# Kernel optimization log

Measured on AMD Instinct MI355X. Metric: run time of the kernel, lower is better.

## Reference

```python
import jax, jax.numpy as jnp
import numpy as np

EMBED_DIM = 1024
NUM_HEADS = 16
HEAD_DIM = EMBED_DIM // NUM_HEADS
BATCH = 2
SEQ = 2048


def setup_inputs() -> dict:
    key = jax.random.key(0)
    ks = jax.random.split(key, 9)
    s = 1.0 / np.sqrt(EMBED_DIM)
    inputs = jax.random.normal(ks[0], (BATCH, SEQ, EMBED_DIM), dtype=jnp.float32)
    Wq = jax.random.normal(ks[1], (EMBED_DIM, EMBED_DIM), dtype=jnp.float32) * s
    bq = jnp.zeros((EMBED_DIM,), dtype=jnp.float32)
    Wk = jax.random.normal(ks[2], (EMBED_DIM, EMBED_DIM), dtype=jnp.float32) * s
    bk = jnp.zeros((EMBED_DIM,), dtype=jnp.float32)
    Wv = jax.random.normal(ks[3], (EMBED_DIM, EMBED_DIM), dtype=jnp.float32) * s
    bv = jnp.zeros((EMBED_DIM,), dtype=jnp.float32)
    Wo = jax.random.normal(ks[4], (EMBED_DIM, EMBED_DIM), dtype=jnp.float32) * s
    bo = jnp.zeros((EMBED_DIM,), dtype=jnp.float32)
    return {"inputs": inputs, "Wq": Wq, "bq": bq, "Wk": Wk, "bk": bk,
            "Wv": Wv, "bv": bv, "Wo": Wo, "bo": bo}


def _split_heads(x):
    # [B, S, D] -> [B, H, S, d]
    b, s, _ = x.shape
    return x.reshape(b, s, NUM_HEADS, HEAD_DIM).transpose(0, 2, 1, 3)


def reference(inputs, Wq, bq, Wk, bk, Wv, bv, Wo, bo):
    q = _split_heads(inputs @ Wq + bq)
    k = _split_heads(inputs @ Wk + bk)
    v = _split_heads(inputs @ Wv + bv)
    scale = 1.0 / jnp.sqrt(jnp.float32(HEAD_DIM))
    # [B, H, Sq, Sk]
    scores = jnp.einsum('bhqd,bhkd->bhqk', q, k) * scale
    weights = jax.nn.softmax(scores, axis=-1)
    attn = jnp.einsum('bhqk,bhkd->bhqd', weights, v)
    # [B, H, S, d] -> [B, S, D]
    b = inputs.shape[0]
    concat = attn.transpose(0, 2, 1, 3).reshape(b, -1, EMBED_DIM)
    output = concat @ Wo + bo
    return (output, weights)
```

## Files before the change

kernel.cpp:

```cpp
#include <hip/hip_runtime.h>

typedef __bf16 bf16;
typedef __bf16 bf16x4 __attribute__((ext_vector_type(4)));
typedef __bf16 bf16x8 __attribute__((ext_vector_type(8)));
typedef float f32x4 __attribute__((ext_vector_type(4)));

#define EMBED 1024
#define SEQ   2048
#define NH    16
#define DH    64
#define MROWS 4096

__device__ __forceinline__ void gload16(const void* g, void* l) {
    __builtin_amdgcn_global_load_lds((const __attribute__((address_space(1))) void*)g,
                                     (__attribute__((address_space(3))) void*)l,
                                     16, 0, 0);
}

__global__ void cvt_x_kernel(const float* __restrict__ x, bf16* __restrict__ xb) {
    int i = (blockIdx.x * 256 + threadIdx.x) * 4;
    float4 v = *(const float4*)(x + i);
    bf16x4 o;
    o[0] = (bf16)v.x; o[1] = (bf16)v.y; o[2] = (bf16)v.z; o[3] = (bf16)v.w;
    *(bf16x4*)(xb + i) = o;
}

__global__ void cvt_wt_kernel(const float* __restrict__ w0, const float* __restrict__ w1,
                              const float* __restrict__ w2, const float* __restrict__ w3,
                              bf16* __restrict__ o0, bf16* __restrict__ o1,
                              bf16* __restrict__ o2, bf16* __restrict__ o3) {
    const float* w; bf16* o;
    switch (blockIdx.z) {
        case 0: w = w0; o = o0; break;
        case 1: w = w1; o = o1; break;
        case 2: w = w2; o = o2; break;
        default: w = w3; o = o3; break;
    }
    __shared__ float t[32][33];
    int tx = threadIdx.x & 31, ty = threadIdx.x >> 5;
    int c0 = blockIdx.x * 32, r0 = blockIdx.y * 32;
    #pragma unroll
    for (int i = 0; i < 32; i += 8)
        t[ty + i][tx] = w[(size_t)(r0 + ty + i) * EMBED + c0 + tx];
    __syncthreads();
    #pragma unroll
    for (int i = 0; i < 32; i += 8)
        o[(size_t)(c0 + ty + i) * EMBED + r0 + tx] = (bf16)t[tx][ty + i];
}

template <bool F32OUT>
__device__ __forceinline__ void gemm_body(const bf16* __restrict__ A,
                                          const bf16* __restrict__ Bm,
                                          const float* __restrict__ bias,
                                          void* __restrict__ Cout) {
    __shared__ bf16 As[128 * 64];
    __shared__ bf16 Bs[128 * 64];
    const int tid = threadIdx.x, wave = tid >> 6, lane = tid & 63;
    const int qd = lane >> 4, ln = lane & 15;
    const int m0 = blockIdx.y * 128, n0 = blockIdx.x * 128;
    const int wr = (wave >> 1) * 64, wc = (wave & 1) * 64;
    const int lrow8 = lane >> 3, lcol8 = (lane & 7) * 8;
    f32x4 acc[4][4] = {};

    for (int k0 = 0; k0 < EMBED; k0 += 64) {
        #pragma unroll
        for (int i = 0; i < 4; ++i) {
            int seg = i * 4 + wave;
            const bf16* ga = A  + (size_t)(m0 + seg * 8 + lrow8) * EMBED + k0 + lcol8;
            const bf16* gb = Bm + (size_t)(n0 + seg * 8 + lrow8) * EMBED + k0 + lcol8;
            gload16(ga, As + seg * 512);
            gload16(gb, Bs + seg * 512);
        }
        __syncthreads();
        #pragma unroll
        for (int kk = 0; kk < 64; kk += 32) {
            bf16x8 af[4], bfr[4];
            #pragma unroll
            for (int mt = 0; mt < 4; ++mt)
                af[mt] = *(const bf16x8*)(As + (wr + mt * 16 + ln) * 64 + kk + qd * 8);
            #pragma unroll
            for (int nt = 0; nt < 4; ++nt)
                bfr[nt] = *(const bf16x8*)(Bs + (wc + nt * 16 + ln) * 64 + kk + qd * 8);
            #pragma unroll
            for (int mt = 0; mt < 4; ++mt)
                #pragma unroll
                for (int nt = 0; nt < 4; ++nt)
                    acc[mt][nt] = __builtin_amdgcn_mfma_f32_16x16x32_bf16(
                        af[mt], bfr[nt], acc[mt][nt], 0, 0, 0);
        }
        __syncthreads();
    }
    #pragma unroll
    for (int mt = 0; mt < 4; ++mt) {
        #pragma unroll
        for (int nt = 0; nt < 4; ++nt) {
            int col = n0 + wc + nt * 16 + ln;
            float bv = bias[col];
            #pragma unroll
            for (int r = 0; r < 4; ++r) {
                int row = m0 + wr + mt * 16 + qd * 4 + r;
                float v = acc[mt][nt][r] + bv;
                if (F32OUT) ((float*)Cout)[(size_t)row * EMBED + col] = v;
                else        ((bf16*)Cout)[(size_t)row * EMBED + col] = (bf16)v;
            }
        }
    }
}

__global__ void gemm_qkv_kernel(const bf16* __restrict__ A,
                                const bf16* __restrict__ B0, const bf16* __restrict__ B1,
                                const bf16* __restrict__ B2,
                                const float* __restrict__ b0, const float* __restrict__ b1,
                                const float* __restrict__ b2,
                                bf16* __restrict__ C0, bf16* __restrict__ C1,
                                bf16* __restrict__ C2) {
    const bf16* Bm; const float* bias; bf16* C;
    switch (blockIdx.z) {
        case 0: Bm = B0; bias = b0; C = C0; break;
        case 1: Bm = B1; bias = b1; C = C1; break;
        default: Bm = B2; bias = b2; C = C2; break;
    }
    gemm_body<false>(A, Bm, bias, (void*)C);
}

__global__ void gemm_o_kernel(const bf16* __restrict__ A, const bf16* __restrict__ Bm,
                              const float* __restrict__ bias, float* __restrict__ C) {
    gemm_body<true>(A, Bm, bias, (void*)C);
}

__global__ void attn_kernel(const bf16* __restrict__ Q, const bf16* __restrict__ K,
                            const bf16* __restrict__ V, float* __restrict__ Wout,
                            bf16* __restrict__ O) {
    const int qb = blockIdx.x;
    const int bh = blockIdx.y;
    const int b = bh >> 4, h = bh & 15;
    const size_t rowbase = (size_t)b * SEQ;
    const int colbase = h * DH;

    __shared__ bf16 Qs[128 * 64];
    __shared__ bf16 Ks[64 * 64];
    __shared__ bf16 Vts[64 * 72];
    __shared__ bf16 Ps[128 * 72];
    __shared__ float rl[128];

    const int tid = threadIdx.x, wave = tid >> 6, lane = tid & 63;
    const int qd = lane >> 4, ln = lane & 15;
    const int lrow8 = lane >> 3, lcol8 = (lane & 7) * 8;
    const float scale = 0.125f;

    #pragma unroll
    for (int i = 0; i < 4; ++i) {
        int seg = i * 4 + wave;
        gload16(Q + (rowbase + qb * 128 + seg * 8 + lrow8) * EMBED + colbase + lcol8,
                Qs + seg * 512);
    }

    float lsum[2][4] = {};

    for (int kb = 0; kb < 32; ++kb) {
        #pragma unroll
        for (int i = 0; i < 2; ++i) {
            int seg = i * 4 + wave;
            gload16(K + (rowbase + kb * 64 + seg * 8 + lrow8) * EMBED + colbase + lcol8,
                    Ks + seg * 512);
        }
        __syncthreads();
        f32x4 sacc[2][4] = {};
        #pragma unroll
        for (int kk = 0; kk < 64; kk += 32) {
            bf16x8 af[2], bfr[4];
            #pragma unroll
            for (int mt = 0; mt < 2; ++mt)
                af[mt] = *(const bf16x8*)(Qs + (wave * 32 + mt * 16 + ln) * 64 + kk + qd * 8);
            #pragma unroll
            for (int nt = 0; nt < 4; ++nt)
                bfr[nt] = *(const bf16x8*)(Ks + (nt * 16 + ln) * 64 + kk + qd * 8);
            #pragma unroll
            for (int mt = 0; mt < 2; ++mt)
                #pragma unroll
                for (int nt = 0; nt < 4; ++nt)
                    sacc[mt][nt] = __builtin_amdgcn_mfma_f32_16x16x32_bf16(
                        af[mt], bfr[nt], sacc[mt][nt], 0, 0, 0);
        }
        #pragma unroll
        for (int mt = 0; mt < 2; ++mt)
            #pragma unroll
            for (int r = 0; r < 4; ++r) {
                float s = 0.f;
                #pragma unroll
                for (int nt = 0; nt < 4; ++nt) s += __expf(sacc[mt][nt][r] * scale);
                lsum[mt][r] += s;
            }
        __syncthreads();
    }
    #pragma unroll
    for (int mt = 0; mt < 2; ++mt)
        #pragma unroll
        for (int r = 0; r < 4; ++r) {
            float s = lsum[mt][r];
            s += __shfl_xor(s, 1); s += __shfl_xor(s, 2);
            s += __shfl_xor(s, 4); s += __shfl_xor(s, 8);
            if (ln == 0) rl[wave * 32 + mt * 16 + qd * 4 + r] = 1.0f / s;
        }

    f32x4 oacc[2][4] = {};
    for (int kb = 0; kb < 32; ++kb) {
        #pragma unroll
        for (int i = 0; i < 2; ++i) {
            int seg = i * 4 + wave;
            gload16(K + (rowbase + kb * 64 + seg * 8 + lrow8) * EMBED + colbase + lcol8,
                    Ks + seg * 512);
        }
        {
            int r = tid >> 2, dg = tid & 3;
            const bf16* vp = V + (rowbase + kb * 64 + r) * EMBED + colbase + dg * 16;
            bf16x8 v0 = *(const bf16x8*)(vp);
            bf16x8 v1 = *(const bf16x8*)(vp + 8);
            #pragma unroll
            for (int j = 0; j < 8; ++j) Vts[(dg * 16 + j) * 72 + r] = v0[j];
            #pragma unroll
            for (int j = 0; j < 8; ++j) Vts[(dg * 16 + 8 + j) * 72 + r] = v1[j];
        }
        __syncthreads();
        f32x4 sacc[2][4] = {};
        #pragma unroll
        for (int kk = 0; kk < 64; kk += 32) {
            bf16x8 af[2], bfr[4];
            #pragma unroll
            for (int mt = 0; mt < 2; ++mt)
                af[mt] = *(const bf16x8*)(Qs + (wave * 32 + mt * 16 + ln) * 64 + kk + qd * 8);
            #pragma unroll
            for (int nt = 0; nt < 4; ++nt)
                bfr[nt] = *(const bf16x8*)(Ks + (nt * 16 + ln) * 64 + kk + qd * 8);
            #pragma unroll
            for (int mt = 0; mt < 2; ++mt)
                #pragma unroll
                for (int nt = 0; nt < 4; ++nt)
                    sacc[mt][nt] = __builtin_amdgcn_mfma_f32_16x16x32_bf16(
                        af[mt], bfr[nt], sacc[mt][nt], 0, 0, 0);
        }
        float* wb = Wout + ((size_t)bh * SEQ + qb * 128) * SEQ + kb * 64;
        #pragma unroll
        for (int mt = 0; mt < 2; ++mt) {
            int lrow = wave * 32 + mt * 16 + qd * 4;
            #pragma unroll
            for (int r = 0; r < 4; ++r) {
                float rli = rl[lrow + r];
                #pragma unroll
                for (int nt = 0; nt < 4; ++nt) {
                    float p = __expf(sacc[mt][nt][r] * scale) * rli;
                    wb[(size_t)(lrow + r) * SEQ + nt * 16 + ln] = p;
                    Ps[(lrow + r) * 72 + nt * 16 + ln] = (bf16)p;
                }
            }
        }
        #pragma unroll
        for (int kk = 0; kk < 64; kk += 32) {
            bf16x8 pf[2], vf[4];
            #pragma unroll
            for (int mt = 0; mt < 2; ++mt)
                pf[mt] = *(const bf16x8*)(Ps + (wave * 32 + mt * 16 + ln) * 72 + kk + qd * 8);
            #pragma unroll
            for (int nt = 0; nt < 4; ++nt)
                vf[nt] = *(const bf16x8*)(Vts + (nt * 16 + ln) * 72 + kk + qd * 8);
            #pragma unroll
            for (int mt = 0; mt < 2; ++mt)
                #pragma unroll
                for (int nt = 0; nt < 4; ++nt)
                    oacc[mt][nt] = __builtin_amdgcn_mfma_f32_16x16x32_bf16(
                        pf[mt], vf[nt], oacc[mt][nt], 0, 0, 0);
        }
        __syncthreads();
    }
    #pragma unroll
    for (int mt = 0; mt < 2; ++mt) {
        int lrow = wave * 32 + mt * 16 + qd * 4;
        #pragma unroll
        for (int nt = 0; nt < 4; ++nt) {
            int d = nt * 16 + ln;
            #pragma unroll
            for (int r = 0; r < 4; ++r)
                O[(rowbase + qb * 128 + lrow + r) * EMBED + colbase + d] = (bf16)oacc[mt][nt][r];
        }
    }
}

extern "C" void kernel_launch(void* const* d_in, const int* in_sizes, int n_in,
                              void* d_out, int out_size, void* d_ws, size_t ws_size,
                              hipStream_t stream) {
    const float* x  = (const float*)d_in[0];
    const float* Wq = (const float*)d_in[1];
    const float* bq = (const float*)d_in[2];
    const float* Wk = (const float*)d_in[3];
    const float* bk = (const float*)d_in[4];
    const float* Wv = (const float*)d_in[5];
    const float* bv = (const float*)d_in[6];
    const float* Wo = (const float*)d_in[7];
    const float* bo = (const float*)d_in[8];

    float* out0 = (float*)d_out;
    float* Wout = (float*)d_out + (size_t)MROWS * EMBED;

    const size_t MB = 1u << 20;
    char* ws = (char*)d_ws;
    bf16* Xb  = (bf16*)(ws + 0 * MB);
    bf16* Wqb = (bf16*)(ws + 8 * MB);
    bf16* Wkb = (bf16*)(ws + 10 * MB);
    bf16* Wvb = (bf16*)(ws + 12 * MB);
    bf16* Wob = (bf16*)(ws + 14 * MB);
    bf16* Qb  = (bf16*)(ws + 16 * MB);
    bf16* Kb  = (bf16*)(ws + 24 * MB);
    bf16* Vb  = (bf16*)(ws + 32 * MB);
    bf16* Ob  = (bf16*)(ws + 40 * MB);

    cvt_x_kernel<<<4096, 256, 0, stream>>>(x, Xb);
    cvt_wt_kernel<<<dim3(32, 32, 4), 256, 0, stream>>>(Wq, Wk, Wv, Wo, Wqb, Wkb, Wvb, Wob);
    gemm_qkv_kernel<<<dim3(8, 32, 3), 256, 0, stream>>>(Xb, Wqb, Wkb, Wvb, bq, bk, bv,
                                                        Qb, Kb, Vb);
    attn_kernel<<<dim3(16, 32), 256, 0, stream>>>(Qb, Kb, Vb, Wout, Ob);
    gemm_o_kernel<<<dim3(8, 32), 256, 0, stream>>>(Ob, Wob, bo, out0);
}
```

Baseline: 727.4 us.

## Split attention into parallel sumexp pass and PV pass with pre-transposed V

Splits the single attention kernel into a sumexp kernel and a PV kernel. The sumexp kernel parallelizes the row-sum of exponentials over key blocks as well, and combines partial sums with atomics into a zeroed buffer. The V projection GEMM now writes V in a per-head transposed layout, so the PV kernel no longer transposes through LDS element by element. The PV kernel uses 64-row query tiles, giving more blocks, and writes the weights with vector stores. The price is extra launches, atomics, and reusing the X workspace region for the sum buffer, which is only safe because the sum buffer is zeroed after the GEMMs have read X.

```diff
diff --git a/kernel.cpp b/kernel.cpp
--- a/kernel.cpp
+++ b/kernel.cpp
@@ -17,7 +17,8 @@
                                      16, 0, 0);
 }
 
-__global__ void cvt_x_kernel(const float* __restrict__ x, bf16* __restrict__ xb) {
+__global__ __launch_bounds__(256) void cvt_x_kernel(const float* __restrict__ x,
+                                                    bf16* __restrict__ xb) {
     int i = (blockIdx.x * 256 + threadIdx.x) * 4;
     float4 v = *(const float4*)(x + i);
     bf16x4 o;
@@ -25,10 +26,11 @@
     *(bf16x4*)(xb + i) = o;
 }
 
-__global__ void cvt_wt_kernel(const float* __restrict__ w0, const float* __restrict__ w1,
-                              const float* __restrict__ w2, const float* __restrict__ w3,
-                              bf16* __restrict__ o0, bf16* __restrict__ o1,
-                              bf16* __restrict__ o2, bf16* __restrict__ o3) {
+__global__ __launch_bounds__(256) void cvt_wt_kernel(
+        const float* __restrict__ w0, const float* __restrict__ w1,
+        const float* __restrict__ w2, const float* __restrict__ w3,
+        bf16* __restrict__ o0, bf16* __restrict__ o1,
+        bf16* __restrict__ o2, bf16* __restrict__ o3) {
     const float* w; bf16* o;
     switch (blockIdx.z) {
         case 0: w = w0; o = o0; break;
@@ -48,7 +50,13 @@
         o[(size_t)(c0 + ty + i) * EMBED + r0 + tx] = (bf16)t[tx][ty + i];
 }
 
-template <bool F32OUT>
+__global__ __launch_bounds__(256) void zero_l_kernel(float* __restrict__ l) {
+    int i = (blockIdx.x * 256 + threadIdx.x) * 4;
+    f32x4 z = {};
+    *(f32x4*)(l + i) = z;
+}
+
+template <int MODE>
 __device__ __forceinline__ void gemm_body(const bf16* __restrict__ A,
                                           const bf16* __restrict__ Bm,
                                           const float* __restrict__ bias,
@@ -90,199 +98,186 @@
         }
         __syncthreads();
     }
-    #pragma unroll
-    for (int mt = 0; mt < 4; ++mt) {
-        #pragma unroll
-        for (int nt = 0; nt < 4; ++nt) {
-            int col = n0 + wc + nt * 16 + ln;
-            float bv = bias[col];
-            #pragma unroll
-            for (int r = 0; r < 4; ++r) {
-                int row = m0 + wr + mt * 16 + qd * 4 + r;
-                float v = acc[mt][nt][r] + bv;
-                if (F32OUT) ((float*)Cout)[(size_t)row * EMBED + col] = v;
-                else        ((bf16*)Cout)[(size_t)row * EMBED + col] = (bf16)v;
-            }
-        }
-    }
-}
-
-__global__ void gemm_qkv_kernel(const bf16* __restrict__ A,
-                                const bf16* __restrict__ B0, const bf16* __restrict__ B1,
-                                const bf16* __restrict__ B2,
-                                const float* __restrict__ b0, const float* __restrict__ b1,
-                                const float* __restrict__ b2,
-                                bf16* __restrict__ C0, bf16* __restrict__ C1,
-                                bf16* __restrict__ C2) {
-    const bf16* Bm; const float* bias; bf16* C;
-    switch (blockIdx.z) {
-        case 0: Bm = B0; bias = b0; C = C0; break;
-        case 1: Bm = B1; bias = b1; C = C1; break;
-        default: Bm = B2; bias = b2; C = C2; break;
-    }
-    gemm_body<false>(A, Bm, bias, (void*)C);
-}
-
-__global__ void gemm_o_kernel(const bf16* __restrict__ A, const bf16* __restrict__ Bm,
-                              const float* __restrict__ bias, float* __restrict__ C) {
-    gemm_body<true>(A, Bm, bias, (void*)C);
-}
-
-__global__ void attn_kernel(const bf16* __restrict__ Q, const bf16* __restrict__ K,
-                            const bf16* __restrict__ V, float* __restrict__ Wout,
-                            bf16* __restrict__ O) {
-    const int qb = blockIdx.x;
-    const int bh = blockIdx.y;
+    if (MODE == 2) {
+        const int b = m0 >> 11;
+        const int sbase = (m0 & 2047) + wr;
+        #pragma unroll
+        for (int mt = 0; mt < 4; ++mt) {
+            #pragma unroll
+            for (int nt = 0; nt < 4; ++nt) {
+                int col = n0 + wc + nt * 16 + ln;
+                int h = col >> 6, d = col & 63;
+                float bv = bias[col];
+                bf16x4 pk;
+                #pragma unroll
+                for (int r = 0; r < 4; ++r) pk[r] = (bf16)(acc[mt][nt][r] + bv);
+                *(bf16x4*)((bf16*)Cout +
+                    ((size_t)(b * NH + h) * DH + d) * SEQ + sbase + mt * 16 + qd * 4) = pk;
+            }
+        }
+    } else {
+        #pragma unroll
+        for (int mt = 0; mt < 4; ++mt) {
+            #pragma unroll
+            for (int nt = 0; nt < 4; ++nt) {
+                int col = n0 + wc + nt * 16 + ln;
+                float bv = bias[col];
+                #pragma unroll
+                for (int r = 0; r < 4; ++r) {
+                    int row = m0 + wr + mt * 16 + qd * 4 + r;
+                    float v = acc[mt][nt][r] + bv;
+                    if (MODE == 1) ((float*)Cout)[(size_t)row * EMBED + col] = v;
+                    else           ((bf16*)Cout)[(size_t)row * EMBED + col] = (bf16)v;
+                }
+            }
+        }
+    }
+}
+
+__global__ __launch_bounds__(256) void gemm_qk_kernel(
+        const bf16* __restrict__ A,
+        const bf16* __restrict__ B0, const bf16* __restrict__ B1,
+        const float* __restrict__ b0, const float* __restrict__ b1,
+        bf16* __restrict__ C0, bf16* __restrict__ C1) {
+    if (blockIdx.z == 0) gemm_body<0>(A, B0, b0, (void*)C0);
+    else                 gemm_body<0>(A, B1, b1, (void*)C1);
+}
+
+__global__ __launch_bounds__(256) void gemm_v_kernel(
+        const bf16* __restrict__ A, const bf16* __restrict__ Bm,
+        const float* __restrict__ bias, bf16* __restrict__ Vt) {
+    gemm_body<2>(A, Bm, bias, (void*)Vt);
+}
+
+__global__ __launch_bounds__(256) void gemm_o_kernel(
+        const bf16* __restrict__ A, const bf16* __restrict__ Bm,
+        const float* __restrict__ bias, float* __restrict__ C) {
+    gemm_body<1>(A, Bm, bias, (void*)C);
+}
+
+__global__ __launch_bounds__(256) void sumexp_kernel(const bf16* __restrict__ Q,
+                                                     const bf16* __restrict__ K,
+                                                     float* __restrict__ l) {
+    const int qb = blockIdx.x, kb = blockIdx.y, bh = blockIdx.z;
     const int b = bh >> 4, h = bh & 15;
     const size_t rowbase = (size_t)b * SEQ;
     const int colbase = h * DH;
-
-    __shared__ bf16 Qs[128 * 64];
-    __shared__ bf16 Ks[64 * 64];
-    __shared__ bf16 Vts[64 * 72];
-    __shared__ bf16 Ps[128 * 72];
-    __shared__ float rl[128];
-
+    __shared__ bf16 Ks[128 * 72];
     const int tid = threadIdx.x, wave = tid >> 6, lane = tid & 63;
     const int qd = lane >> 4, ln = lane & 15;
-    const int lrow8 = lane >> 3, lcol8 = (lane & 7) * 8;
-    const float scale = 0.125f;
-
-    #pragma unroll
-    for (int i = 0; i < 4; ++i) {
-        int seg = i * 4 + wave;
-        gload16(Q + (rowbase + qb * 128 + seg * 8 + lrow8) * EMBED + colbase + lcol8,
-                Qs + seg * 512);
-    }
-
-    float lsum[2][4] = {};
+    {
+        int row = tid >> 1, c0 = (tid & 1) * 32;
+        const bf16* kp = K + (rowbase + kb * 128 + row) * EMBED + colbase + c0;
+        #pragma unroll
+        for (int j = 0; j < 4; ++j)
+            *(bf16x8*)(Ks + row * 72 + c0 + j * 8) = *(const bf16x8*)(kp + j * 8);
+    }
+    __syncthreads();
+    bf16x8 qf[2][2];
+    #pragma unroll
+    for (int ni = 0; ni < 2; ++ni)
+        #pragma unroll
+        for (int kkid = 0; kkid < 2; ++kkid)
+            qf[ni][kkid] = *(const bf16x8*)(
+                Q + (rowbase + qb * 128 + wave * 32 + ni * 16 + ln) * EMBED +
+                colbase + kkid * 32 + qd * 8);
+    float ssum[2] = {0.f, 0.f};
+    #pragma unroll
+    for (int mi = 0; mi < 8; ++mi) {
+        bf16x8 kf[2];
+        #pragma unroll
+        for (int kkid = 0; kkid < 2; ++kkid)
+            kf[kkid] = *(const bf16x8*)(Ks + (mi * 16 + ln) * 72 + kkid * 32 + qd * 8);
+        #pragma unroll
+        for (int ni = 0; ni < 2; ++ni) {
+            f32x4 acc = {};
+            acc = __builtin_amdgcn_mfma_f32_16x16x32_bf16(kf[0], qf[ni][0], acc, 0, 0, 0);
+            acc = __builtin_amdgcn_mfma_f32_16x16x32_bf16(kf[1], qf[ni][1], acc, 0, 0, 0);
+            #pragma unroll
+            for (int r = 0; r < 4; ++r) ssum[ni] += __expf(acc[r] * 0.125f);
+        }
+    }
+    #pragma unroll
+    for (int ni = 0; ni < 2; ++ni) {
+        float s = ssum[ni];
+        s += __shfl_xor(s, 16);
+        s += __shfl_xor(s, 32);
+        if (lane < 16)
+            atomicAdd(l + (size_t)bh * SEQ + qb * 128 + wave * 32 + ni * 16 + ln, s);
+    }
+}
+
+__global__ __launch_bounds__(256) void attn_pv_kernel(
+        const bf16* __restrict__ Q, const bf16* __restrict__ K,
+        const bf16* __restrict__ Vt, const float* __restrict__ l,
+        float* __restrict__ Wout, bf16* __restrict__ O) {
+    const int qb = blockIdx.x, bh = blockIdx.y;
+    const int b = bh >> 4, h = bh & 15;
+    const size_t rowbase = (size_t)b * SEQ;
+    const int colbase = h * DH;
+    __shared__ bf16 Ks[64 * 72];
+    __shared__ bf16 Vts[64 * 72];
+    __shared__ bf16 Pt[64 * 72];
+    const int tid = threadIdx.x, wave = tid >> 6, lane = tid & 63;
+    const int qd = lane >> 4, ln = lane & 15;
+    const int qrow = qb * 64 + wave * 16 + ln;
+
+    bf16x8 qf[2];
+    qf[0] = *(const bf16x8*)(Q + (rowbase + qrow) * EMBED + colbase + qd * 8);
+    qf[1] = *(const bf16x8*)(Q + (rowbase + qrow) * EMBED + colbase + 32 + qd * 8);
+    const float rl = 1.0f / l[(size_t)bh * SEQ + qrow];
+
+    f32x4 oacc[4] = {};
+    const int srow = tid >> 2, sc = (tid & 3) * 16;
+    const bf16* kp = K + (rowbase + srow) * EMBED + colbase + sc;
+    const bf16* vp = Vt + ((size_t)bh * DH + srow) * SEQ + sc;
+    float* wrow = Wout + ((size_t)bh * SEQ + qrow) * SEQ;
 
     for (int kb = 0; kb < 32; ++kb) {
-        #pragma unroll
-        for (int i = 0; i < 2; ++i) {
-            int seg = i * 4 + wave;
-            gload16(K + (rowbase + kb * 64 + seg * 8 + lrow8) * EMBED + colbase + lcol8,
-                    Ks + seg * 512);
-        }
+        bf16x8 k0 = *(const bf16x8*)(kp + (size_t)kb * 64 * EMBED);
+        bf16x8 k1 = *(const bf16x8*)(kp + (size_t)kb * 64 * EMBED + 8);
+        bf16x8 v0 = *(const bf16x8*)(vp + kb * 64);
+        bf16x8 v1 = *(const bf16x8*)(vp + kb * 64 + 8);
+        *(bf16x8*)(Ks + srow * 72 + sc) = k0;
+        *(bf16x8*)(Ks + srow * 72 + sc + 8) = k1;
+        *(bf16x8*)(Vts + srow * 72 + sc) = v0;
+        *(bf16x8*)(Vts + srow * 72 + sc + 8) = v1;
         __syncthreads();
-        f32x4 sacc[2][4] = {};
-        #pragma unroll
-        for (int kk = 0; kk < 64; kk += 32) {
-            bf16x8 af[2], bfr[4];
-            #pragma unroll
-            for (int mt = 0; mt < 2; ++mt)
-                af[mt] = *(const bf16x8*)(Qs + (wave * 32 + mt * 16 + ln) * 64 + kk + qd * 8);
-            #pragma unroll
-            for (int nt = 0; nt < 4; ++nt)
-                bfr[nt] = *(const bf16x8*)(Ks + (nt * 16 + ln) * 64 + kk + qd * 8);
-            #pragma unroll
-            for (int mt = 0; mt < 2; ++mt)
-                #pragma unroll
-                for (int nt = 0; nt < 4; ++nt)
-                    sacc[mt][nt] = __builtin_amdgcn_mfma_f32_16x16x32_bf16(
-                        af[mt], bfr[nt], sacc[mt][nt], 0, 0, 0);
-        }
-        #pragma unroll
-        for (int mt = 0; mt < 2; ++mt)
+        #pragma unroll
+        for (int mi = 0; mi < 4; ++mi) {
+            f32x4 acc = {};
+            #pragma unroll
+            for (int kkid = 0; kkid < 2; ++kkid) {
+                bf16x8 kf = *(const bf16x8*)(Ks + (mi * 16 + ln) * 72 + kkid * 32 + qd * 8);
+                acc = __builtin_amdgcn_mfma_f32_16x16x32_bf16(kf, qf[kkid], acc, 0, 0, 0);
+            }
+            float4 pw; bf16x4 pb;
             #pragma unroll
             for (int r = 0; r < 4; ++r) {
-                float s = 0.f;
-                #pragma unroll
-                for (int nt = 0; nt < 4; ++nt) s += __expf(sacc[mt][nt][r] * scale);
-                lsum[mt][r] += s;
-            }
+                float p = __expf(acc[r] * 0.125f) * rl;
+                ((float*)&pw)[r] = p;
+                pb[r] = (bf16)p;
+            }
+            *(float4*)(wrow + kb * 64 + mi * 16 + qd * 4) = pw;
+            *(bf16x4*)(Pt + (wave * 16 + ln) * 72 + mi * 16 + qd * 4) = pb;
+        }
+        #pragma unroll
+        for (int kkid = 0; kkid < 2; ++kkid) {
+            bf16x8 pf = *(const bf16x8*)(Pt + (wave * 16 + ln) * 72 + kkid * 32 + qd * 8);
+            #pragma unroll
+            for (int ni = 0; ni < 4; ++ni) {
+                bf16x8 vf = *(const bf16x8*)(Vts + (ni * 16 + ln) * 72 + kkid * 32 + qd * 8);
+                oacc[ni] = __builtin_amdgcn_mfma_f32_16x16x32_bf16(pf, vf, oacc[ni], 0, 0, 0);
+            }
+        }
         __syncthreads();
     }
     #pragma unroll
-    for (int mt = 0; mt < 2; ++mt)
-        #pragma unroll
-        for (int r = 0; r < 4; ++r) {
-            float s = lsum[mt][r];
-            s += __shfl_xor(s, 1); s += __shfl_xor(s, 2);
-            s += __shfl_xor(s, 4); s += __shfl_xor(s, 8);
-            if (ln == 0) rl[wave * 32 + mt * 16 + qd * 4 + r] = 1.0f / s;
-        }
-
-    f32x4 oacc[2][4] = {};
-    for (int kb = 0; kb < 32; ++kb) {
-        #pragma unroll
-        for (int i = 0; i < 2; ++i) {
-            int seg = i * 4 + wave;
-            gload16(K + (rowbase + kb * 64 + seg * 8 + lrow8) * EMBED + colbase + lcol8,
-                    Ks + seg * 512);
-        }
-        {
-            int r = tid >> 2, dg = tid & 3;
-            const bf16* vp = V + (rowbase + kb * 64 + r) * EMBED + colbase + dg * 16;
-            bf16x8 v0 = *(const bf16x8*)(vp);
-            bf16x8 v1 = *(const bf16x8*)(vp + 8);
-            #pragma unroll
-            for (int j = 0; j < 8; ++j) Vts[(dg * 16 + j) * 72 + r] = v0[j];
-            #pragma unroll
-            for (int j = 0; j < 8; ++j) Vts[(dg * 16 + 8 + j) * 72 + r] = v1[j];
-        }
-        __syncthreads();
-        f32x4 sacc[2][4] = {};
-        #pragma unroll
-        for (int kk = 0; kk < 64; kk += 32) {
-            bf16x8 af[2], bfr[4];
-            #pragma unroll
-            for (int mt = 0; mt < 2; ++mt)
-                af[mt] = *(const bf16x8*)(Qs + (wave * 32 + mt * 16 + ln) * 64 + kk + qd * 8);
-            #pragma unroll
-            for (int nt = 0; nt < 4; ++nt)
-                bfr[nt] = *(const bf16x8*)(Ks + (nt * 16 + ln) * 64 + kk + qd * 8);
-            #pragma unroll
-            for (int mt = 0; mt < 2; ++mt)
-                #pragma unroll
-                for (int nt = 0; nt < 4; ++nt)
-                    sacc[mt][nt] = __builtin_amdgcn_mfma_f32_16x16x32_bf16(
-                        af[mt], bfr[nt], sacc[mt][nt], 0, 0, 0);
-        }
-        float* wb = Wout + ((size_t)bh * SEQ + qb * 128) * SEQ + kb * 64;
-        #pragma unroll
-        for (int mt = 0; mt < 2; ++mt) {
-            int lrow = wave * 32 + mt * 16 + qd * 4;
-            #pragma unroll
-            for (int r = 0; r < 4; ++r) {
-                float rli = rl[lrow + r];
-                #pragma unroll
-                for (int nt = 0; nt < 4; ++nt) {
-                    float p = __expf(sacc[mt][nt][r] * scale) * rli;
-                    wb[(size_t)(lrow + r) * SEQ + nt * 16 + ln] = p;
-                    Ps[(lrow + r) * 72 + nt * 16 + ln] = (bf16)p;
-                }
-            }
-        }
-        #pragma unroll
-        for (int kk = 0; kk < 64; kk += 32) {
-            bf16x8 pf[2], vf[4];
-            #pragma unroll
-            for (int mt = 0; mt < 2; ++mt)
-                pf[mt] = *(const bf16x8*)(Ps + (wave * 32 + mt * 16 + ln) * 72 + kk + qd * 8);
-            #pragma unroll
-            for (int nt = 0; nt < 4; ++nt)
-                vf[nt] = *(const bf16x8*)(Vts + (nt * 16 + ln) * 72 + kk + qd * 8);
-            #pragma unroll
-            for (int mt = 0; mt < 2; ++mt)
-                #pragma unroll
-                for (int nt = 0; nt < 4; ++nt)
-                    oacc[mt][nt] = __builtin_amdgcn_mfma_f32_16x16x32_bf16(
-                        pf[mt], vf[nt], oacc[mt][nt], 0, 0, 0);
-        }
-        __syncthreads();
-    }
-    #pragma unroll
-    for (int mt = 0; mt < 2; ++mt) {
-        int lrow = wave * 32 + mt * 16 + qd * 4;
-        #pragma unroll
-        for (int nt = 0; nt < 4; ++nt) {
-            int d = nt * 16 + ln;
-            #pragma unroll
-            for (int r = 0; r < 4; ++r)
-                O[(rowbase + qb * 128 + lrow + r) * EMBED + colbase + d] = (bf16)oacc[mt][nt][r];
-        }
-    }
+    for (int ni = 0; ni < 4; ++ni)
+        #pragma unroll
+        for (int r = 0; r < 4; ++r)
+            O[(rowbase + qb * 64 + wave * 16 + qd * 4 + r) * EMBED + colbase + ni * 16 + ln] =
+                (bf16)oacc[ni][r];
 }
 
 extern "C" void kernel_launch(void* const* d_in, const int* in_sizes, int n_in,
@@ -303,20 +298,23 @@
 
     const size_t MB = 1u << 20;
     char* ws = (char*)d_ws;
-    bf16* Xb  = (bf16*)(ws + 0 * MB);
-    bf16* Wqb = (bf16*)(ws + 8 * MB);
-    bf16* Wkb = (bf16*)(ws + 10 * MB);
-    bf16* Wvb = (bf16*)(ws + 12 * MB);
-    bf16* Wob = (bf16*)(ws + 14 * MB);
-    bf16* Qb  = (bf16*)(ws + 16 * MB);
-    bf16* Kb  = (bf16*)(ws + 24 * MB);
-    bf16* Vb  = (bf16*)(ws + 32 * MB);
-    bf16* Ob  = (bf16*)(ws + 40 * MB);
+    bf16*  Xb  = (bf16*)(ws + 0 * MB);
+    float* lb  = (float*)(ws + 0 * MB);
+    bf16*  Wqb = (bf16*)(ws + 8 * MB);
+    bf16*  Wkb = (bf16*)(ws + 10 * MB);
+    bf16*  Wvb = (bf16*)(ws + 12 * MB);
+    bf16*  Wob = (bf16*)(ws + 14 * MB);
+    bf16*  Qb  = (bf16*)(ws + 16 * MB);
+    bf16*  Kb  = (bf16*)(ws + 24 * MB);
+    bf16*  Vt  = (bf16*)(ws + 32 * MB);
+    bf16*  Ob  = (bf16*)(ws + 40 * MB);
 
     cvt_x_kernel<<<4096, 256, 0, stream>>>(x, Xb);
     cvt_wt_kernel<<<dim3(32, 32, 4), 256, 0, stream>>>(Wq, Wk, Wv, Wo, Wqb, Wkb, Wvb, Wob);
-    gemm_qkv_kernel<<<dim3(8, 32, 3), 256, 0, stream>>>(Xb, Wqb, Wkb, Wvb, bq, bk, bv,
-                                                        Qb, Kb, Vb);
-    attn_kernel<<<dim3(16, 32), 256, 0, stream>>>(Qb, Kb, Vb, Wout, Ob);
+    gemm_qk_kernel<<<dim3(8, 32, 2), 256, 0, stream>>>(Xb, Wqb, Wkb, bq, bk, Qb, Kb);
+    gemm_v_kernel<<<dim3(8, 32), 256, 0, stream>>>(Xb, Wvb, bv, Vt);
+    zero_l_kernel<<<64, 256, 0, stream>>>(lb);
+    sumexp_kernel<<<dim3(16, 16, 32), 256, 0, stream>>>(Qb, Kb, lb);
+    attn_pv_kernel<<<dim3(32, 32), 256, 0, stream>>>(Qb, Kb, Vt, lb, Wout, Ob);
     gemm_o_kernel<<<dim3(8, 32), 256, 0, stream>>>(Ob, Wob, bo, out0);
 }
```

New measurement: 790.7 us. +8.7%, slower.
